# Performance work log

Measured on AMD Instinct MI355X. Metric: run time of the kernel, lower is better.

## Reference

```python
import jax, jax.numpy as jnp
from jax import lax
import numpy as np

RATE = 6.0          # self.rate buffer
STRIDE = 1
PAD = 1
DIL = 1
R_BLUR = 2          # gaussian blur radius for sigma=1.0 (5x5 kernel)


def _unit_circle():
    # 3x3 kernel taps: center (0,0), 8 outer taps normalized to the unit circle. (y, x) order.
    pts = []
    for ky in (-1.0, 0.0, 1.0):
        for kx in (-1.0, 0.0, 1.0):
            n = np.hypot(ky, kx)
            pts.append([ky / n, kx / n] if n > 0 else [0.0, 0.0])
    return jnp.asarray(np.array(pts, np.float32))  # (9, 2)

UNIT_CIRCLE = _unit_circle()


def blur2d_sphere(x, sigma):
    # Isotropic gaussian blur, depthwise, SAME padding. Kernel values depend on traced sigma.
    c = jnp.arange(-R_BLUR, R_BLUR + 1, dtype=x.dtype)
    g = jnp.exp(-(c[:, None] ** 2 + c[None, :] ** 2) / (2.0 * sigma * sigma))
    g = g / g.sum()
    C = x.shape[1]
    k = jnp.broadcast_to(g[None, None], (C, 1, 2 * R_BLUR + 1, 2 * R_BLUR + 1))
    return lax.conv_general_dilated(x, k, (1, 1), [(R_BLUR, R_BLUR)] * 2,
                                    feature_group_count=C)


def _axis_sample(x, pos, axis, size):
    # 1D linear interpolation gather along `axis` at fractional positions `pos`;
    # out-of-range corners contribute zero (deform_conv semantics).
    dt = x.dtype
    p0 = jnp.floor(pos)
    t = (pos - p0).astype(dt)
    i0 = p0.astype(jnp.int32)
    i1 = i0 + 1
    w0 = (1.0 - t) * ((i0 >= 0) & (i0 < size)).astype(dt)
    w1 = t * ((i1 >= 0) & (i1 < size)).astype(dt)
    g0 = jnp.take(x, jnp.clip(i0, 0, size - 1), axis=axis)
    g1 = jnp.take(x, jnp.clip(i1, 0, size - 1), axis=axis)
    sh = [1, 1, 1, 1]
    sh[axis] = -1
    return w0.reshape(sh) * g0 + w1.reshape(sh) * g1


def _forward(x, sigma, weight):
    x = blur2d_sphere(x, sigma)
    B, C, H, W = x.shape
    O = weight.shape[0]
    off = UNIT_CIRCLE.astype(x.dtype) * (sigma * RATE)  # (9, 2): per-tap (dy, dx), constant over b,h,w
    Ho = (H + 2 * PAD - DIL * 2 - 1) // STRIDE + 1
    Wo = (W + 2 * PAD - DIL * 2 - 1) // STRIDE + 1
    base_y = jnp.arange(Ho, dtype=x.dtype) * STRIDE - PAD
    base_x = jnp.arange(Wo, dtype=x.dtype) * STRIDE - PAD
    wflat = weight.reshape(O, C, 9)
    out = jnp.zeros((B, O, Ho, Wo), x.dtype)
    # Offsets are spatially constant, so deformable bilinear sampling is separable per tap.
    for ky in range(3):
        for kx in range(3):
            k = ky * 3 + kx
            py = base_y + (ky * DIL) + off[k, 0]   # (Ho,)
            px = base_x + (kx * DIL) + off[k, 1]   # (Wo,)
            xr = _axis_sample(x, py, 2, H)          # (B, C, Ho, W)
            v = _axis_sample(xr, px, 3, W)          # (B, C, Ho, Wo)
            out = out + jnp.einsum('bchw,oc->bohw', v, wflat[:, :, k])
    return out


def setup_inputs() -> dict:
    key = jax.random.key(0)
    k1, k2 = jax.random.split(key)
    x = jax.random.normal(k1, (16, 32, 256, 256), jnp.float32)
    fan_in = 32 * 9
    fan_out = 32 * 9
    limit = float(np.sqrt(6.0 / (fan_in + fan_out)))  # xavier_uniform
    weight = jax.random.uniform(k2, (32, 32, 3, 3), jnp.float32, -limit, limit)
    sigma = jnp.float32(1.0)
    return {"x": x, "sigma": sigma, "weight": weight}


def reference(x, sigma, weight):
    return _forward(x, sigma, weight)
```

## Files before the change

### kernel.cpp

```cpp
#include <hip/hip_runtime.h>
#include <math.h>

#define BB 16
#define CC 32
#define OO 32
#define HH 256
#define WW 256
#define HW (HH * WW)
#define PD 8
#define HP (HH + 2 * PD)
#define WP (WW + 2 * PD)
#define NEMAX 36

#define MWROWS 22
#define MRUNITS 192
#define MWUNITS (MWROWS * MRUNITS)

typedef __attribute__((ext_vector_type(8))) short bf16x8;
typedef __attribute__((ext_vector_type(4))) float f32x4;
typedef __attribute__((ext_vector_type(4))) unsigned short us4;
typedef __attribute__((ext_vector_type(8))) unsigned short us8;

__device__ __forceinline__ unsigned short f2bf(float f) {
    unsigned u = __float_as_uint(f);
    u += 0x7fffu + ((u >> 16) & 1u);
    return (unsigned short)(u >> 16);
}
__device__ __forceinline__ float bf2f(unsigned short v) {
    return __uint_as_float((unsigned)v << 16);
}

__device__ __forceinline__ void blur_wn(const float* sigma_p, float* wn) {
    const float sigma = sigma_p[0];
    const float inv2s2 = 1.0f / (2.0f * sigma * sigma);
    float e[5], s = 0.0f;
#pragma unroll
    for (int i = 0; i < 5; ++i) {
        float d = (float)(i - 2);
        e[i] = expf(-(d * d) * inv2s2);
        s += e[i];
    }
    const float inv_s = 1.0f / s;
#pragma unroll
    for (int i = 0; i < 5; ++i) wn[i] = e[i] * inv_s;
}

__global__ __launch_bounds__(256) void blur_t_kernel(const float* __restrict__ x,
                                                     const float* __restrict__ sigma_p,
                                                     unsigned short* __restrict__ xbt) {
    __shared__ __align__(16) unsigned short vb[16][2][268];
    const int t     = threadIdx.x;
    const int blk   = ((blockIdx.x & 7) << 9) + (blockIdx.x >> 3);
    const int chalf = blk & 1;
    const int band  = (blk >> 1) & 127;
    const int b     = blk >> 8;
    const int h0    = band << 1;

    float wn[5];
    blur_wn(sigma_p, wn);

    unsigned short* xb_img = xbt + (size_t)b * (HP * WP * CC);

    const us8 z8 = {0, 0, 0, 0, 0, 0, 0, 0};
    if (t < 64) {
        const int j  = t >> 5;
        const int px = (t >> 1) & 15;
        const int ch = t & 1;
        const int xx = (px < PD) ? px : px + WW;
        *reinterpret_cast<us8*>(xb_img + ((size_t)(h0 + PD + j) * WP + xx) * CC
                                + chalf * 16 + ch * 8) = z8;
    }
    if (h0 < PD) {
#pragma unroll
        for (int j2 = 0; j2 < 2; ++j2) {
            unsigned short* dst = xb_img + (size_t)(h0 + j2) * WP * CC + chalf * 16;
            for (int i = t; i < WP * 2; i += 256)
                *reinterpret_cast<us8*>(dst + (size_t)(i >> 1) * CC + (i & 1) * 8) = z8;
        }
    }
#pragma unroll
    for (int j2 = 0; j2 < 2; ++j2) {
        if (h0 + j2 >= HH - PD) {
            unsigned short* dst = xb_img + (size_t)(h0 + j2 + 2 * PD) * WP * CC + chalf * 16;
            for (int i = t; i < WP * 2; i += 256)
                *reinterpret_cast<us8*>(dst + (size_t)(i >> 1) * CC + (i & 1) * 8) = z8;
        }
    }

    if (t < 128) {
        const int cl = t >> 3;
        const int j  = (t >> 2) & 1;
        const int e_ = t & 3;
        const int idx = (e_ < 2) ? (2 + e_) : (258 + e_);
        vb[cl][j][idx] = 0;
    }

    const int g  = t & 63;
    const int wv = t >> 6;
#pragma unroll
    for (int it = 0; it < 4; ++it) {
        const int cl = (it << 2) + wv;
        const int c  = chalf * 16 + cl;
        const float* xc = x + ((size_t)(b * CC + c) * HH) * WW + 4 * g;
        f32x4 v[6];
#pragma unroll
        for (int k = 0; k < 6; ++k) {
            const int r = h0 - 2 + k;
            v[k] = (r >= 0 && r < HH)
                 ? *reinterpret_cast<const f32x4*>(xc + r * WW)
                 : (f32x4){0.f, 0.f, 0.f, 0.f};
        }
#pragma unroll
        for (int j = 0; j < 2; ++j) {
            f32x4 a = {0.f, 0.f, 0.f, 0.f};
#pragma unroll
            for (int i = 0; i < 5; ++i) {
                a[0] = fmaf(wn[i], v[j + i][0], a[0]);
                a[1] = fmaf(wn[i], v[j + i][1], a[1]);
                a[2] = fmaf(wn[i], v[j + i][2], a[2]);
                a[3] = fmaf(wn[i], v[j + i][3], a[3]);
            }
            us4 bv;
            bv[0] = f2bf(a[0]); bv[1] = f2bf(a[1]);
            bv[2] = f2bf(a[2]); bv[3] = f2bf(a[3]);
            *reinterpret_cast<us4*>(&vb[cl][j][4 + 4 * g]) = bv;
        }
    }
    __syncthreads();

    const int cu8 = t & 1;
    const int p4  = (t >> 1) & 63;
    const int j   = t >> 7;
    const int P   = p4 << 2;
    const int cl0 = cu8 << 3;

    us8 o[4];
#pragma unroll
    for (int cc = 0; cc < 8; ++cc) {
        const unsigned short* vp = &vb[cl0 + cc][j][P];
        us4 r0 = *reinterpret_cast<const us4*>(vp);
        us4 r1 = *reinterpret_cast<const us4*>(vp + 4);
        us4 r2 = *reinterpret_cast<const us4*>(vp + 8);
        float v[12];
#pragma unroll
        for (int q = 0; q < 4; ++q) {
            v[q] = bf2f(r0[q]); v[4 + q] = bf2f(r1[q]); v[8 + q] = bf2f(r2[q]);
        }
#pragma unroll
        for (int d = 0; d < 4; ++d) {
            float a = 0.0f;
#pragma unroll
            for (int i = 0; i < 5; ++i) a = fmaf(wn[i], v[d + 2 + i], a);
            o[d][cc] = f2bf(a);
        }
    }
    unsigned short* obj = xb_img + ((size_t)(h0 + PD + j) * WP + PD + P) * CC
                                 + chalf * 16 + cl0;
#pragma unroll
    for (int d = 0; d < 4; ++d)
        *reinterpret_cast<us8*>(obj + d * CC) = o[d];
}

__global__ void wtrans_kernel(const float* __restrict__ wgt,
                              const float* __restrict__ sigma_p,
                              int* __restrict__ meta,
                              unsigned short* __restrict__ wb2) {
    __shared__ int   s_tap[36];
    __shared__ float s_w[36];
    __shared__ int   s_soff[36];
    __shared__ int   s_wrel[36];
    __shared__ int   s_n;
    const int t = threadIdx.x;

    if (t == 0) {
        const float UY[9] = {-0.70710678f, -1.0f, -0.70710678f, 0.0f, 0.0f, 0.0f,
                              0.70710678f,  1.0f,  0.70710678f};
        const float UX[9] = {-0.70710678f, 0.0f, 0.70710678f, -1.0f, 0.0f, 1.0f,
                             -0.70710678f, 0.0f, 0.70710678f};
        const int KYI[9] = {-1, -1, -1, 0, 0, 0, 1, 1, 1};
        const int KXI[9] = {-1, 0, 1, -1, 0, 1, -1, 0, 1};
        const float s6 = sigma_p[0] * 6.0f;
        int n = 0, ok = 1;
        for (int s_ = 0; s_ < 9; ++s_) {
            float offy = UY[s_] * s6, offx = UX[s_] * s6;
            float fy = floorf(offy), fx = floorf(offx);
            float ty = offy - fy,    tx = offx - fx;
            int sy = KYI[s_] + (int)fy;
            int sx = KXI[s_] + (int)fx;
            float wy[2] = {1.0f - ty, ty};
            float wx[2] = {1.0f - tx, tx};
            for (int dy = 0; dy < 2; ++dy)
                for (int dx = 0; dx < 2; ++dx) {
                    float wc = wy[dy] * wx[dx];
                    if (wc != 0.0f) {
                        const int syc = sy + dy, sxc = sx + dx;
                        s_tap[n]  = s_;
                        s_w[n]    = wc;
                        s_soff[n] = (syc * WP + sxc) * CC;
                        s_wrel[n] = (syc + 7) * MRUNITS + (sxc + 8) * 4;
                        if (syc < -7 || syc > 7 || sxc < -7 || sxc > 7) ok = 0;
                        ++n;
                    }
                }
        }
        for (int i = 1; i < n; ++i) {
            int ks = s_soff[i]; int kt = s_tap[i]; float kw = s_w[i]; int kr = s_wrel[i];
            int j = i - 1;
            while (j >= 0 && s_soff[j] > ks) {
                s_soff[j + 1] = s_soff[j]; s_tap[j + 1] = s_tap[j];
                s_w[j + 1] = s_w[j];       s_wrel[j + 1] = s_wrel[j];
                --j;
            }
            s_soff[j + 1] = ks; s_tap[j + 1] = kt; s_w[j + 1] = kw; s_wrel[j + 1] = kr;
        }
        if (blockIdx.x == 0) {
            meta[0] = n;
            for (int i = 0; i < n; ++i) { meta[1 + i] = s_soff[i]; meta[37 + i] = s_wrel[i]; }
            meta[74] = ok;
        }
        s_n = n;
    }
    __syncthreads();

    const int e = blockIdx.x;
    if (e >= s_n) return;
    for (int i = t; i < 1024; i += 256) {
        int j  = i & 7;
        int l  = (i >> 3) & 63;
        int nh = (i >> 9) & 1;
        int o  = nh * 16 + (l & 15);
        int c  = ((l >> 4) << 3) + j;
        wb2[e * 1024 + i] = f2bf(s_w[e] * wgt[(o * CC + c) * 9 + s_tap[e]]);
    }
}

__global__ __launch_bounds__(512) void mix9_kernel(const unsigned short* __restrict__ xbt,
                                                   const int* __restrict__ meta,
                                                   const unsigned short* __restrict__ wb2,
                                                   float* __restrict__ out) {
    __shared__ bf16x8 win[MWUNITS];
    const int t    = threadIdx.x;
    const int lane = t & 63;
    const int wv   = t >> 6;
    const int blk  = ((blockIdx.x & 7) << 9) + (blockIdx.x >> 3);
    const int xs   = blk & 7;
    const int band = (blk >> 3) & 31;
    const int b    = blk >> 8;
    const int h0   = band << 3;
    const int x0   = xs << 5;
    const int mrow = lane & 15;
    const int cu   = lane >> 4;
    const int ncorn = meta[0];
    const int ok    = meta[74];

    const unsigned short* img = xbt + (size_t)b * (HP * WP * CC);

    f32x4 acc[2][2];
#pragma unroll
    for (int q = 0; q < 2; ++q) {
        acc[q][0] = (f32x4){0.f, 0.f, 0.f, 0.f};
        acc[q][1] = (f32x4){0.f, 0.f, 0.f, 0.f};
    }

    if (ok) {
        const us8* imgu  = reinterpret_cast<const us8*>(img);
        const int  gbase = ((h0 + 1) * WP + x0) * 4;
        for (int i = t; i < MWUNITS; i += 512) {
            const int row = i / MRUNITS;
            const int u   = i - row * MRUNITS;
            reinterpret_cast<us8*>(win)[i] = imgu[gbase + row * (WP * 4) + u];
        }
        __syncthreads();

        const int ubase = wv * MRUNITS + mrow * 4 + cu;
        for (int e = 0; e < ncorn; ++e) {
            const int ewr = meta[37 + e];
            const bf16x8 b0 = *reinterpret_cast<const bf16x8*>(wb2 + ((e * 2 + 0) * 64 + lane) * 8);
            const bf16x8 b1 = *reinterpret_cast<const bf16x8*>(wb2 + ((e * 2 + 1) * 64 + lane) * 8);
            const int abase = ubase + ewr;
#pragma unroll
            for (int tx = 0; tx < 2; ++tx) {
                const bf16x8 a = win[abase + tx * 64];
                acc[tx][0] = __builtin_amdgcn_mfma_f32_16x16x32_bf16(a, b0, acc[tx][0], 0, 0, 0);
                acc[tx][1] = __builtin_amdgcn_mfma_f32_16x16x32_bf16(a, b1, acc[tx][1], 0, 0, 0);
            }
        }
    } else {
        const unsigned short* gb = img + ((size_t)(h0 + wv + PD) * WP + x0 + PD) * CC
                                       + mrow * CC + cu * 8;
        for (int e = 0; e < ncorn; ++e) {
            const int soff = meta[1 + e];
            const bf16x8 b0 = *reinterpret_cast<const bf16x8*>(wb2 + ((e * 2 + 0) * 64 + lane) * 8);
            const bf16x8 b1 = *reinterpret_cast<const bf16x8*>(wb2 + ((e * 2 + 1) * 64 + lane) * 8);
#pragma unroll
            for (int tx = 0; tx < 2; ++tx) {
                const bf16x8 a = *reinterpret_cast<const bf16x8*>(gb + soff + tx * 16 * CC);
                acc[tx][0] = __builtin_amdgcn_mfma_f32_16x16x32_bf16(a, b0, acc[tx][0], 0, 0, 0);
                acc[tx][1] = __builtin_amdgcn_mfma_f32_16x16x32_bf16(a, b1, acc[tx][1], 0, 0, 0);
            }
        }
    }

    const int prow = cu << 2;
    float* opr = out + ((size_t)b * OO + (lane & 15)) * HW + (size_t)(h0 + wv) * WW + x0 + prow;
#pragma unroll
    for (int tx = 0; tx < 2; ++tx) {
        *reinterpret_cast<f32x4*>(opr + tx * 16) = acc[tx][0];
        *reinterpret_cast<f32x4*>(opr + tx * 16 + (size_t)16 * HW) = acc[tx][1];
    }
}

extern "C" void kernel_launch(void* const* d_in, const int* in_sizes, int n_in,
                              void* d_out, int out_size, void* d_ws, size_t ws_size,
                              hipStream_t stream) {
    const float* x     = (const float*)d_in[0];
    const float* sigma = (const float*)d_in[1];
    const float* wgt   = (const float*)d_in[2];
    float* out = (float*)d_out;

    int* meta           = (int*)d_ws;
    unsigned short* wb2 = (unsigned short*)((char*)d_ws + 512);
    unsigned short* xbt = (unsigned short*)((char*)d_ws + 131072);

    wtrans_kernel<<<36, 256, 0, stream>>>(wgt, sigma, meta, wb2);
    blur_t_kernel<<<BB * 256, 256, 0, stream>>>(x, sigma, xbt);
    mix9_kernel<<<BB * 256, 512, 0, stream>>>(xbt, meta, wb2, out);
}
```

Baseline: 152.2 us.

## Blend bilinear corners in registers before MFMA, one matmul per tap

```diff
diff --git a/kernel.cpp b/kernel.cpp
--- a/kernel.cpp
+++ b/kernel.cpp
@@ -168,7 +168,6 @@
     __shared__ int   s_tap[36];
     __shared__ float s_w[36];
     __shared__ int   s_soff[36];
-    __shared__ int   s_wrel[36];
     __shared__ int   s_n;
     const int t = threadIdx.x;
 
@@ -189,6 +188,11 @@
             int sx = KXI[s_] + (int)fx;
             float wy[2] = {1.0f - ty, ty};
             float wx[2] = {1.0f - tx, tx};
+            meta[200 + s_] = (sy + 7) * MRUNITS + (sx + 8) * 4;
+            meta[210 + s_] = __float_as_int(wy[0] * wx[0]);
+            meta[220 + s_] = __float_as_int(wy[0] * wx[1]);
+            meta[230 + s_] = __float_as_int(wy[1] * wx[0]);
+            meta[240 + s_] = __float_as_int(wy[1] * wx[1]);
             for (int dy = 0; dy < 2; ++dy)
                 for (int dx = 0; dx < 2; ++dx) {
                     float wc = wy[dy] * wx[dx];
@@ -197,47 +201,45 @@
                         s_tap[n]  = s_;
                         s_w[n]    = wc;
                         s_soff[n] = (syc * WP + sxc) * CC;
-                        s_wrel[n] = (syc + 7) * MRUNITS + (sxc + 8) * 4;
                         if (syc < -7 || syc > 7 || sxc < -7 || sxc > 7) ok = 0;
                         ++n;
                     }
                 }
         }
-        for (int i = 1; i < n; ++i) {
-            int ks = s_soff[i]; int kt = s_tap[i]; float kw = s_w[i]; int kr = s_wrel[i];
-            int j = i - 1;
-            while (j >= 0 && s_soff[j] > ks) {
-                s_soff[j + 1] = s_soff[j]; s_tap[j + 1] = s_tap[j];
-                s_w[j + 1] = s_w[j];       s_wrel[j + 1] = s_wrel[j];
-                --j;
-            }
-            s_soff[j + 1] = ks; s_tap[j + 1] = kt; s_w[j + 1] = kw; s_wrel[j + 1] = kr;
-        }
-        if (blockIdx.x == 0) {
-            meta[0] = n;
-            for (int i = 0; i < n; ++i) { meta[1 + i] = s_soff[i]; meta[37 + i] = s_wrel[i]; }
-            meta[74] = ok;
-        }
+        meta[0] = n;
+        for (int i = 0; i < n; ++i) meta[1 + i] = s_soff[i];
+        meta[74] = ok;
         s_n = n;
     }
     __syncthreads();
 
     const int e = blockIdx.x;
-    if (e >= s_n) return;
-    for (int i = t; i < 1024; i += 256) {
-        int j  = i & 7;
-        int l  = (i >> 3) & 63;
-        int nh = (i >> 9) & 1;
-        int o  = nh * 16 + (l & 15);
-        int c  = ((l >> 4) << 3) + j;
-        wb2[e * 1024 + i] = f2bf(s_w[e] * wgt[(o * CC + c) * 9 + s_tap[e]]);
-    }
-}
-
-__global__ __launch_bounds__(512) void mix9_kernel(const unsigned short* __restrict__ xbt,
-                                                   const int* __restrict__ meta,
-                                                   const unsigned short* __restrict__ wb2,
-                                                   float* __restrict__ out) {
+    if (e < 9) {
+        for (int i = t; i < 1024; i += 256) {
+            int j  = i & 7;
+            int l  = (i >> 3) & 63;
+            int nh = (i >> 9) & 1;
+            int o  = nh * 16 + (l & 15);
+            int c  = ((l >> 4) << 3) + j;
+            wb2[e * 1024 + i] = f2bf(wgt[(o * CC + c) * 9 + e]);
+        }
+    } else if (e - 9 < s_n) {
+        const int le = e - 9;
+        for (int i = t; i < 1024; i += 256) {
+            int j  = i & 7;
+            int l  = (i >> 3) & 63;
+            int nh = (i >> 9) & 1;
+            int o  = nh * 16 + (l & 15);
+            int c  = ((l >> 4) << 3) + j;
+            wb2[16384 + le * 1024 + i] = f2bf(s_w[le] * wgt[(o * CC + c) * 9 + s_tap[le]]);
+        }
+    }
+}
+
+__global__ __launch_bounds__(512) void mix10_kernel(const unsigned short* __restrict__ xbt,
+                                                    const int* __restrict__ meta,
+                                                    const unsigned short* __restrict__ wb2,
+                                                    float* __restrict__ out) {
     __shared__ bf16x8 win[MWUNITS];
     const int t    = threadIdx.x;
     const int lane = t & 63;
@@ -263,6 +265,13 @@
     }
 
     if (ok) {
+        bf16x8 bt0[9], bt1[9];
+#pragma unroll
+        for (int s = 0; s < 9; ++s) {
+            bt0[s] = *reinterpret_cast<const bf16x8*>(wb2 + ((s * 2 + 0) * 64 + lane) * 8);
+            bt1[s] = *reinterpret_cast<const bf16x8*>(wb2 + ((s * 2 + 1) * 64 + lane) * 8);
+        }
+
         const us8* imgu  = reinterpret_cast<const us8*>(img);
         const int  gbase = ((h0 + 1) * WP + x0) * 4;
         for (int i = t; i < MWUNITS; i += 512) {
@@ -273,30 +282,63 @@
         __syncthreads();
 
         const int ubase = wv * MRUNITS + mrow * 4 + cu;
-        for (int e = 0; e < ncorn; ++e) {
-            const int ewr = meta[37 + e];
-            const bf16x8 b0 = *reinterpret_cast<const bf16x8*>(wb2 + ((e * 2 + 0) * 64 + lane) * 8);
-            const bf16x8 b1 = *reinterpret_cast<const bf16x8*>(wb2 + ((e * 2 + 1) * 64 + lane) * 8);
-            const int abase = ubase + ewr;
-#pragma unroll
-            for (int tx = 0; tx < 2; ++tx) {
-                const bf16x8 a = win[abase + tx * 64];
-                acc[tx][0] = __builtin_amdgcn_mfma_f32_16x16x32_bf16(a, b0, acc[tx][0], 0, 0, 0);
-                acc[tx][1] = __builtin_amdgcn_mfma_f32_16x16x32_bf16(a, b1, acc[tx][1], 0, 0, 0);
+#pragma unroll
+        for (int s = 0; s < 9; ++s) {
+            const int   ab0 = ubase + meta[200 + s];
+            const float w00 = __int_as_float(meta[210 + s]);
+            const float w01 = __int_as_float(meta[220 + s]);
+            const float w10 = __int_as_float(meta[230 + s]);
+            const float w11 = __int_as_float(meta[240 + s]);
+            const bool  bx  = (w01 != 0.0f) || (w11 != 0.0f);
+            const bool  by  = (w10 != 0.0f) || (w11 != 0.0f);
+#pragma unroll
+            for (int tx2 = 0; tx2 < 2; ++tx2) {
+                const int ab = ab0 + tx2 * 64;
+                float v[8];
+                {
+                    const bf16x8 a00 = win[ab];
+#pragma unroll
+                    for (int j = 0; j < 8; ++j)
+                        v[j] = w00 * bf2f((unsigned short)a00[j]);
+                }
+                if (bx) {
+                    const bf16x8 a01 = win[ab + 4];
+#pragma unroll
+                    for (int j = 0; j < 8; ++j)
+                        v[j] = fmaf(w01, bf2f((unsigned short)a01[j]), v[j]);
+                }
+                if (by) {
+                    const bf16x8 a10 = win[ab + MRUNITS];
+#pragma unroll
+                    for (int j = 0; j < 8; ++j)
+                        v[j] = fmaf(w10, bf2f((unsigned short)a10[j]), v[j]);
+                    if (bx) {
+                        const bf16x8 a11 = win[ab + MRUNITS + 4];
+#pragma unroll
+                        for (int j = 0; j < 8; ++j)
+                            v[j] = fmaf(w11, bf2f((unsigned short)a11[j]), v[j]);
+                    }
+                }
+                bf16x8 af;
+#pragma unroll
+                for (int j = 0; j < 8; ++j) af[j] = (short)f2bf(v[j]);
+                acc[tx2][0] = __builtin_amdgcn_mfma_f32_16x16x32_bf16(af, bt0[s], acc[tx2][0], 0, 0, 0);
+                acc[tx2][1] = __builtin_amdgcn_mfma_f32_16x16x32_bf16(af, bt1[s], acc[tx2][1], 0, 0, 0);
             }
         }
     } else {
+        const unsigned short* wb2g = wb2 + 16384;
         const unsigned short* gb = img + ((size_t)(h0 + wv + PD) * WP + x0 + PD) * CC
                                        + mrow * CC + cu * 8;
         for (int e = 0; e < ncorn; ++e) {
             const int soff = meta[1 + e];
-            const bf16x8 b0 = *reinterpret_cast<const bf16x8*>(wb2 + ((e * 2 + 0) * 64 + lane) * 8);
-            const bf16x8 b1 = *reinterpret_cast<const bf16x8*>(wb2 + ((e * 2 + 1) * 64 + lane) * 8);
-#pragma unroll
-            for (int tx = 0; tx < 2; ++tx) {
-                const bf16x8 a = *reinterpret_cast<const bf16x8*>(gb + soff + tx * 16 * CC);
-                acc[tx][0] = __builtin_amdgcn_mfma_f32_16x16x32_bf16(a, b0, acc[tx][0], 0, 0, 0);
-                acc[tx][1] = __builtin_amdgcn_mfma_f32_16x16x32_bf16(a, b1, acc[tx][1], 0, 0, 0);
+            const bf16x8 b0 = *reinterpret_cast<const bf16x8*>(wb2g + ((e * 2 + 0) * 64 + lane) * 8);
+            const bf16x8 b1 = *reinterpret_cast<const bf16x8*>(wb2g + ((e * 2 + 1) * 64 + lane) * 8);
+#pragma unroll
+            for (int tx2 = 0; tx2 < 2; ++tx2) {
+                const bf16x8 a = *reinterpret_cast<const bf16x8*>(gb + soff + tx2 * 16 * CC);
+                acc[tx2][0] = __builtin_amdgcn_mfma_f32_16x16x32_bf16(a, b0, acc[tx2][0], 0, 0, 0);
+                acc[tx2][1] = __builtin_amdgcn_mfma_f32_16x16x32_bf16(a, b1, acc[tx2][1], 0, 0, 0);
             }
         }
     }
@@ -304,9 +346,9 @@
     const int prow = cu << 2;
     float* opr = out + ((size_t)b * OO + (lane & 15)) * HW + (size_t)(h0 + wv) * WW + x0 + prow;
 #pragma unroll
-    for (int tx = 0; tx < 2; ++tx) {
-        *reinterpret_cast<f32x4*>(opr + tx * 16) = acc[tx][0];
-        *reinterpret_cast<f32x4*>(opr + tx * 16 + (size_t)16 * HW) = acc[tx][1];
+    for (int tx2 = 0; tx2 < 2; ++tx2) {
+        *reinterpret_cast<f32x4*>(opr + tx2 * 16) = acc[tx2][0];
+        *reinterpret_cast<f32x4*>(opr + tx2 * 16 + (size_t)16 * HW) = acc[tx2][1];
     }
 }
 
@@ -319,10 +361,10 @@
     float* out = (float*)d_out;
 
     int* meta           = (int*)d_ws;
-    unsigned short* wb2 = (unsigned short*)((char*)d_ws + 512);
+    unsigned short* wb2 = (unsigned short*)((char*)d_ws + 2048);
     unsigned short* xbt = (unsigned short*)((char*)d_ws + 131072);
 
-    wtrans_kernel<<<36, 256, 0, stream>>>(wgt, sigma, meta, wb2);
+    wtrans_kernel<<<45, 256, 0, stream>>>(wgt, sigma, meta, wb2);
     blur_t_kernel<<<BB * 256, 256, 0, stream>>>(x, sigma, xbt);
-    mix9_kernel<<<BB * 256, 512, 0, stream>>>(xbt, meta, wb2, out);
-}
+    mix10_kernel<<<BB * 256, 512, 0, stream>>>(xbt, meta, wb2, out);
+}
```

New measurement: 152.5 us. About the same (+0.2%).
